# Performance work log

Hardware: AMD Instinct MI355X
Metric: run time of the kernel (lower is better)

## Reference

```python
import jax, jax.numpy as jnp
import numpy as np

N_FFT = 1024
HOP = 256
CACHE = N_FFT - 1  # causal left padding
EPS = 1e-12
BATCH = 16
SAMPLES = HOP * 2048


def _make_weight():
    # DFT basis modulated by a periodic Hann window (torch.hann_window default).
    n = np.arange(N_FFT, dtype=np.float32)
    k = np.arange(N_FFT // 2 + 1, dtype=np.float32)[:, None]
    ang = (-2.0 * np.pi / N_FFT) * k * n[None, :]
    win = 0.5 * (1.0 - np.cos(2.0 * np.pi * n / N_FFT))
    w = np.concatenate([np.cos(ang), np.sin(ang)], axis=0) * win  # [2*(N//2+1), N_FFT]
    return jnp.asarray(w, dtype=jnp.float32)[:, None, :]  # [O, I=1, K]


def setup_inputs() -> dict:
    key = jax.random.key(0)
    x = jax.random.normal(key, (BATCH, SAMPLES), dtype=jnp.float32)
    return {"x": x, "weight": _make_weight()}


def reference(x, weight):
    if x.ndim == 2:
        x = x[:, None, :]  # [B, 1, T]
    # causal constant (zero) padding on the left
    x = jnp.pad(x, ((0, 0), (0, 0), (CACHE, 0)))
    # strided conv against the fixed DFT basis: [B, 2*(N//2+1), L]
    y = jax.lax.conv_general_dilated(
        x, weight, window_strides=(HOP,), padding='VALID',
        dimension_numbers=('NCH', 'OIH', 'NCH'))
    B, C, T = y.shape
    y = y.reshape(B, 2, C // 2, T)  # real/imag split
    mag = jnp.sqrt(jnp.clip(jnp.sum(y * y, axis=1), EPS, None))  # [B, N//2+1, L]
    return mag
```

## Files before the change

### kernel.cpp

```cpp
#include <hip/hip_runtime.h>
#include <stdint.h>

#define SAMPLES   524288
#define BATCH     16
#define T_FRAMES  2048
#define K_FFT     1024
#define HOPSZ     256
#define CACHEPAD  1023
#define NCH       513
#define NCH_PAD   576
#define XROW      525312

typedef __bf16          bf16x8 __attribute__((ext_vector_type(8)));
typedef float           f32x4  __attribute__((ext_vector_type(4)));
typedef unsigned short  u16x8  __attribute__((ext_vector_type(8)));

__device__ __forceinline__ unsigned short f2bf(float f) {
    union { float f; unsigned u; } v; v.f = f;
    unsigned r = v.u + 0x7fffu + ((v.u >> 16) & 1u);
    return (unsigned short)(r >> 16);
}

__global__ void x2bf(const float* __restrict__ x, unsigned short* __restrict__ Xb) {
    int bat = blockIdx.y;
    unsigned short* xbo = Xb + (long long)bat * XROW;
    if (blockIdx.x == 0) {
        for (int j = threadIdx.x; j < CACHEPAD; j += 256) xbo[j] = 0;
        xbo[XROW - 1] = 0;
    }
    int i0 = (blockIdx.x * 256 + threadIdx.x) * 8;
    if (i0 >= SAMPLES) return;
    const float* xb = x + (long long)bat * SAMPLES;
    f32x4 a = *(const f32x4*)&xb[i0];
    f32x4 b = *(const f32x4*)&xb[i0 + 4];
    unsigned short* dst = xbo + CACHEPAD + i0;
    #pragma unroll
    for (int e = 0; e < 4; ++e) dst[e]     = f2bf(a[e]);
    #pragma unroll
    for (int e = 0; e < 4; ++e) dst[4 + e] = f2bf(b[e]);
}

__global__ void weight_prep(const float* __restrict__ w, unsigned short* __restrict__ Wb) {
    int i = blockIdx.x * blockDim.x + threadIdx.x;
    int k = i & 1023;
    int c = (i >> 10) % NCH_PAD;
    int s = i / (NCH_PAD * 1024);
    if (s >= 2) return;
    float v = (c < NCH) ? w[((long long)(s * NCH + c)) * K_FFT + k] : 0.f;
    Wb[i] = f2bf(v);
}

__device__ __forceinline__ void gll16(const unsigned short* g, unsigned short* s) {
    __builtin_amdgcn_global_load_lds(
        (const __attribute__((address_space(1))) void*)g,
        (__attribute__((address_space(3))) void*)s,
        16, 0, 0);
}

__global__ __launch_bounds__(256, 3)
void stft_gemm(const unsigned short* __restrict__ Xb,
               const unsigned short* __restrict__ Wb,
               float* __restrict__ out) {
    __shared__ unsigned short Ws[128 * 64];
    __shared__ unsigned short Fs[128 * 64];

    const int id  = blockIdx.x;
    const int xcd = id & 7;
    const int idx = id >> 3;
    const int nt  = idx >> 5;
    const int ft  = (xcd << 5) | (idx & 31);

    const int tid = threadIdx.x;
    const int l   = tid & 63;
    const int w   = tid >> 6;
    const int ln  = l & 15;
    const int qd  = l >> 4;

    const int b  = ft >> 4;
    const int t0 = (ft & 15) * 128;

    const unsigned short* xbase = Xb + (long long)b * XROW;

    const int srow   = l >> 3;
    const int schunk = l & 7;

    const unsigned short* fsrc[4];
    const unsigned short* wsrc[4];
    unsigned short* fdst[4];
    unsigned short* wdst[4];
    #pragma unroll
    for (int c = 0; c < 4; ++c) {
        int r = w * 32 + c * 8 + srow;
        int gchunk = schunk ^ (r & 7);
        fsrc[c] = xbase + (t0 + r) * HOPSZ + gchunk * 8;
        int sel = (r >> 4) & 1;
        int chl = ((r >> 5) << 4) | (r & 15);
        int ch  = nt * 64 + chl;
        wsrc[c] = Wb + ((long long)(sel * NCH_PAD + ch)) * K_FFT + gchunk * 8;
        fdst[c] = Fs + (w * 32 + c * 8) * 64;
        wdst[c] = Ws + (w * 32 + c * 8) * 64;
    }

    const int wave_m = w & 1;
    const int wave_n = w >> 1;

    f32x4 acc[4][4];
    #pragma unroll
    for (int i = 0; i < 4; ++i)
        #pragma unroll
        for (int j = 0; j < 4; ++j)
            acc[i][j] = (f32x4){0.f, 0.f, 0.f, 0.f};

    int a_off[4][2], b_off[4][2];
    #pragma unroll
    for (int i = 0; i < 4; ++i)
        #pragma unroll
        for (int k2 = 0; k2 < 2; ++k2) {
            int ck = ((k2 * 4 + qd) ^ (ln & 7)) * 8;
            a_off[i][k2] = (wave_m * 64 + i * 16 + ln) * 64 + ck;
            b_off[i][k2] = (wave_n * 64 + i * 16 + ln) * 64 + ck;
        }

    for (int kk = 0; kk < K_FFT; kk += 64) {
        #pragma unroll
        for (int c = 0; c < 4; ++c) gll16(fsrc[c] + kk, fdst[c]);
        #pragma unroll
        for (int c = 0; c < 4; ++c) gll16(wsrc[c] + kk, wdst[c]);
        __syncthreads();

        #pragma unroll
        for (int k2 = 0; k2 < 2; ++k2) {
            bf16x8 av[4], bv[4];
            #pragma unroll
            for (int i = 0; i < 4; ++i) av[i] = *(const bf16x8*)&Ws[a_off[i][k2]];
            #pragma unroll
            for (int j = 0; j < 4; ++j) bv[j] = *(const bf16x8*)&Fs[b_off[j][k2]];
            #pragma unroll
            for (int i = 0; i < 4; ++i)
                #pragma unroll
                for (int j = 0; j < 4; ++j)
                    acc[i][j] = __builtin_amdgcn_mfma_f32_16x16x32_bf16(av[i], bv[j], acc[i][j], 0, 0, 0);
        }
        __syncthreads();
    }

    #pragma unroll
    for (int p = 0; p < 2; ++p) {
        #pragma unroll
        for (int j = 0; j < 4; ++j) {
            #pragma unroll
            for (int r = 0; r < 4; ++r) {
                float re  = acc[2 * p][j][r];
                float im  = acc[2 * p + 1][j][r];
                float mag = sqrtf(fmaxf(re * re + im * im, 1e-12f));
                int ch = nt * 64 + (wave_m * 2 + p) * 16 + qd * 4 + r;
                int t  = t0 + wave_n * 64 + j * 16 + ln;
                if (ch < NCH)
                    out[((long long)b * NCH + ch) * T_FRAMES + t] = mag;
            }
        }
    }
}

extern "C" void kernel_launch(void* const* d_in, const int* in_sizes, int n_in,
                              void* d_out, int out_size, void* d_ws, size_t ws_size,
                              hipStream_t stream) {
    const float* x  = (const float*)d_in[0];
    const float* wt = (const float*)d_in[1];
    float* out = (float*)d_out;

    unsigned short* Xb = (unsigned short*)d_ws;
    unsigned short* Wb = (unsigned short*)((char*)d_ws + (size_t)33554432);

    dim3 xgrid(SAMPLES / (256 * 8), 16);
    x2bf<<<xgrid, 256, 0, stream>>>(x, Xb);
    weight_prep<<<4608, 256, 0, stream>>>(wt, Wb);
    stft_gemm<<<dim3(2304), 256, 0, stream>>>(Xb, Wb, out);
}
```

Baseline: 162.4 us.

## Fuse prep kernels, vectorize conversion, load frame operand directly from global

The two preprocessing kernels are merged into one launch, and the conversion now writes 16-byte vectors, reading 8 fp32 values per thread for both x and the weights. In the GEMM, the frame (B) operand is no longer staged through LDS. Each lane loads its bf16x8 fragments straight from global memory, where they come from overlapping frames and are likely cache-resident, and the B LDS buffer is dropped. This removes one launch, halves LDS use and cuts LDS traffic, but adds global-load latency inside the k-loop before the barrier.

```diff
diff --git a/kernel.cpp b/kernel.cpp
--- a/kernel.cpp
+++ b/kernel.cpp
@@ -10,6 +10,9 @@
 #define NCH       513
 #define NCH_PAD   576
 #define XROW      525312
+#define XCHUNKS   (XROW / 8)
+#define XBLOCKS   (257 * BATCH)
+#define WBLOCKS   576
 
 typedef __bf16          bf16x8 __attribute__((ext_vector_type(8)));
 typedef float           f32x4  __attribute__((ext_vector_type(4)));
@@ -21,33 +24,53 @@
     return (unsigned short)(r >> 16);
 }
 
-__global__ void x2bf(const float* __restrict__ x, unsigned short* __restrict__ Xb) {
-    int bat = blockIdx.y;
-    unsigned short* xbo = Xb + (long long)bat * XROW;
-    if (blockIdx.x == 0) {
-        for (int j = threadIdx.x; j < CACHEPAD; j += 256) xbo[j] = 0;
-        xbo[XROW - 1] = 0;
-    }
-    int i0 = (blockIdx.x * 256 + threadIdx.x) * 8;
-    if (i0 >= SAMPLES) return;
-    const float* xb = x + (long long)bat * SAMPLES;
-    f32x4 a = *(const f32x4*)&xb[i0];
-    f32x4 b = *(const f32x4*)&xb[i0 + 4];
-    unsigned short* dst = xbo + CACHEPAD + i0;
-    #pragma unroll
-    for (int e = 0; e < 4; ++e) dst[e]     = f2bf(a[e]);
-    #pragma unroll
-    for (int e = 0; e < 4; ++e) dst[4 + e] = f2bf(b[e]);
-}
-
-__global__ void weight_prep(const float* __restrict__ w, unsigned short* __restrict__ Wb) {
-    int i = blockIdx.x * blockDim.x + threadIdx.x;
-    int k = i & 1023;
-    int c = (i >> 10) % NCH_PAD;
-    int s = i / (NCH_PAD * 1024);
-    if (s >= 2) return;
-    float v = (c < NCH) ? w[((long long)(s * NCH + c)) * K_FFT + k] : 0.f;
-    Wb[i] = f2bf(v);
+__global__ void prep(const float* __restrict__ x, const float* __restrict__ w,
+                     unsigned short* __restrict__ Xb, unsigned short* __restrict__ Wb) {
+    int bid = blockIdx.x;
+    if (bid < XBLOCKS) {
+        int bat = bid / 257;
+        int blk = bid % 257;
+        int j = blk * 256 + threadIdx.x;
+        if (j >= XCHUNKS) return;
+        const float* xb = x + (long long)bat * SAMPLES;
+        unsigned short* xbo = Xb + (long long)bat * XROW;
+        int o0 = j * 8;
+        u16x8 v;
+        if (j >= 128 && j <= 65537) {
+            const float* p = xb + (o0 - 1024);
+            f32x4 A  = *(const f32x4*)p;
+            f32x4 Bv = *(const f32x4*)(p + 4);
+            f32x4 C  = *(const f32x4*)(p + 8);
+            v[0] = f2bf(A[1]);  v[1] = f2bf(A[2]);  v[2] = f2bf(A[3]);
+            v[3] = f2bf(Bv[0]); v[4] = f2bf(Bv[1]); v[5] = f2bf(Bv[2]);
+            v[6] = f2bf(Bv[3]); v[7] = f2bf(C[0]);
+        } else {
+            #pragma unroll
+            for (int e = 0; e < 8; ++e) {
+                int s = o0 + e - CACHEPAD;
+                v[e] = (s >= 0 && s < SAMPLES) ? f2bf(xb[s]) : (unsigned short)0;
+            }
+        }
+        *(u16x8*)&xbo[o0] = v;
+    } else {
+        int i = (bid - XBLOCKS) * 256 + threadIdx.x;
+        int k0 = (i & 127) * 8;
+        int c  = (i >> 7) % NCH_PAD;
+        int s  = i / (NCH_PAD * 128);
+        if (s >= 2) return;
+        u16x8 v;
+        if (c < NCH) {
+            const float* p = w + ((long long)(s * NCH + c)) * K_FFT + k0;
+            f32x4 A  = *(const f32x4*)p;
+            f32x4 Bv = *(const f32x4*)(p + 4);
+            #pragma unroll
+            for (int e = 0; e < 4; ++e) { v[e] = f2bf(A[e]); v[4 + e] = f2bf(Bv[e]); }
+        } else {
+            #pragma unroll
+            for (int e = 0; e < 8; ++e) v[e] = 0;
+        }
+        *(u16x8*)&Wb[((long long)(s * NCH_PAD + c)) * K_FFT + k0] = v;
+    }
 }
 
 __device__ __forceinline__ void gll16(const unsigned short* g, unsigned short* s) {
@@ -62,7 +85,6 @@
                const unsigned short* __restrict__ Wb,
                float* __restrict__ out) {
     __shared__ unsigned short Ws[128 * 64];
-    __shared__ unsigned short Fs[128 * 64];
 
     const int id  = blockIdx.x;
     const int xcd = id & 7;
@@ -83,27 +105,27 @@
 
     const int srow   = l >> 3;
     const int schunk = l & 7;
-
-    const unsigned short* fsrc[4];
     const unsigned short* wsrc[4];
-    unsigned short* fdst[4];
     unsigned short* wdst[4];
     #pragma unroll
     for (int c = 0; c < 4; ++c) {
         int r = w * 32 + c * 8 + srow;
         int gchunk = schunk ^ (r & 7);
-        fsrc[c] = xbase + (t0 + r) * HOPSZ + gchunk * 8;
         int sel = (r >> 4) & 1;
         int chl = ((r >> 5) << 4) | (r & 15);
         int ch  = nt * 64 + chl;
         wsrc[c] = Wb + ((long long)(sel * NCH_PAD + ch)) * K_FFT + gchunk * 8;
-        fdst[c] = Fs + (w * 32 + c * 8) * 64;
         wdst[c] = Ws + (w * 32 + c * 8) * 64;
     }
 
     const int wave_m = w & 1;
     const int wave_n = w >> 1;
 
+    const unsigned short* bbase[4];
+    #pragma unroll
+    for (int j = 0; j < 4; ++j)
+        bbase[j] = xbase + (long long)(t0 + wave_n * 64 + j * 16 + ln) * HOPSZ + qd * 8;
+
     f32x4 acc[4][4];
     #pragma unroll
     for (int i = 0; i < 4; ++i)
@@ -111,35 +133,38 @@
         for (int j = 0; j < 4; ++j)
             acc[i][j] = (f32x4){0.f, 0.f, 0.f, 0.f};
 
-    int a_off[4][2], b_off[4][2];
+    int a_off[4][2];
     #pragma unroll
     for (int i = 0; i < 4; ++i)
         #pragma unroll
         for (int k2 = 0; k2 < 2; ++k2) {
             int ck = ((k2 * 4 + qd) ^ (ln & 7)) * 8;
             a_off[i][k2] = (wave_m * 64 + i * 16 + ln) * 64 + ck;
-            b_off[i][k2] = (wave_n * 64 + i * 16 + ln) * 64 + ck;
         }
 
     for (int kk = 0; kk < K_FFT; kk += 64) {
         #pragma unroll
-        for (int c = 0; c < 4; ++c) gll16(fsrc[c] + kk, fdst[c]);
-        #pragma unroll
         for (int c = 0; c < 4; ++c) gll16(wsrc[c] + kk, wdst[c]);
+
+        bf16x8 bv[2][4];
+        #pragma unroll
+        for (int k2 = 0; k2 < 2; ++k2)
+            #pragma unroll
+            for (int j = 0; j < 4; ++j)
+                bv[k2][j] = *(const bf16x8*)(bbase[j] + kk + k2 * 32);
+
         __syncthreads();
 
         #pragma unroll
         for (int k2 = 0; k2 < 2; ++k2) {
-            bf16x8 av[4], bv[4];
+            bf16x8 av[4];
             #pragma unroll
             for (int i = 0; i < 4; ++i) av[i] = *(const bf16x8*)&Ws[a_off[i][k2]];
-            #pragma unroll
-            for (int j = 0; j < 4; ++j) bv[j] = *(const bf16x8*)&Fs[b_off[j][k2]];
             #pragma unroll
             for (int i = 0; i < 4; ++i)
                 #pragma unroll
                 for (int j = 0; j < 4; ++j)
-                    acc[i][j] = __builtin_amdgcn_mfma_f32_16x16x32_bf16(av[i], bv[j], acc[i][j], 0, 0, 0);
+                    acc[i][j] = __builtin_amdgcn_mfma_f32_16x16x32_bf16(av[i], bv[k2][j], acc[i][j], 0, 0, 0);
         }
         __syncthreads();
     }
@@ -172,8 +197,6 @@
     unsigned short* Xb = (unsigned short*)d_ws;
     unsigned short* Wb = (unsigned short*)((char*)d_ws + (size_t)33554432);
 
-    dim3 xgrid(SAMPLES / (256 * 8), 16);
-    x2bf<<<xgrid, 256, 0, stream>>>(x, Xb);
-    weight_prep<<<4608, 256, 0, stream>>>(wt, Wb);
+    prep<<<XBLOCKS + WBLOCKS, 256, 0, stream>>>(x, wt, Xb, Wb);
     stft_gemm<<<dim3(2304), 256, 0, stream>>>(Xb, Wb, out);
 }
```

After: 241.5 us. 48.7% more time.
